# Kernel tuning notes

Measured on AMD Instinct MI355X. Metric: run time of the kernel, lower is better.

## Reference

```python
import jax, jax.numpy as jnp
import numpy as np

L, N, E, H = 1024, 8, 1024, 16
D = E // H

def setup_inputs() -> dict:
    key = jax.random.key(0)
    k1, k2, k3 = jax.random.split(key, 3)
    x = jax.random.normal(k1, (L, N, E), dtype=jnp.float32)
    # xavier-uniform-like scale for in_proj_weight (3E x E)
    bound = float(np.sqrt(6.0 / (3 * E + E)))
    in_proj_weight = jax.random.uniform(k2, (3 * E, E), dtype=jnp.float32, minval=-bound, maxval=bound)
    in_proj_bias = jnp.zeros((3 * E,), dtype=jnp.float32)
    wb = float(np.sqrt(1.0 / E))
    out_w = jax.random.uniform(k3, (E, E), dtype=jnp.float32, minval=-wb, maxval=wb)
    out_b = jnp.zeros((E,), dtype=jnp.float32)
    return {"x": x, "in_proj_weight": in_proj_weight, "in_proj_bias": in_proj_bias,
            "out_w": out_w, "out_b": out_b}

def reference(x, in_proj_weight, in_proj_bias, out_w, out_b):
    # self-attention: query == key == value == x, stacked input projection
    stack = x @ in_proj_weight.T + in_proj_bias          # L x N x 3E
    q, k, v = jnp.split(stack, 3, axis=-1)               # each L x N x E
    q = q.reshape(L, N, H, D)
    k = k.reshape(L, N, H, D)
    v = v.reshape(L, N, H, D)
    logit = jnp.einsum('lnhd,snhd->lnhs', q, k) / jnp.sqrt(jnp.float32(D))
    weight = jax.nn.softmax(logit, axis=-1)              # L x N x H x S
    context = jnp.einsum('lnhs,snhd->lnhd', weight, v)   # L x N x H x D
    context = context.reshape(L, N, E) @ out_w.T + out_b # L x N x E
    attn = jnp.transpose(weight.mean(axis=-2), (1, 0, 2))  # N x L x S
    return context, attn
```

## Files before the change

### kernel.cpp

```cpp
#include <hip/hip_runtime.h>
#include <stdint.h>

#define LL 1024
#define NB 8
#define EE 1024
#define HH 16
#define DD 64
#define MM (LL*NB)
#define K3 (3*EE)

typedef __attribute__((ext_vector_type(8))) short bf16x8;
typedef __attribute__((ext_vector_type(4))) float f32x4;
typedef __attribute__((ext_vector_type(4))) unsigned short u16x4;
typedef __attribute__((ext_vector_type(8))) unsigned short u16x8;

__device__ __forceinline__ unsigned short f2bf(float f) {
  uint32_t u = __builtin_bit_cast(uint32_t, f);
  u += 0x7fffu + ((u >> 16) & 1u);
  return (unsigned short)(u >> 16);
}
__device__ __forceinline__ uint32_t cvtpk(float lo, float hi) {
  uint32_t d;
  asm volatile("v_cvt_pk_bf16_f32 %0, %1, %2" : "=v"(d) : "v"(lo), "v"(hi));
  return d;
}
__device__ __forceinline__ f32x4 mfma16(bf16x8 a, bf16x8 b, f32x4 c) {
  return __builtin_amdgcn_mfma_f32_16x16x32_bf16(a, b, c, 0, 0, 0);
}
__device__ __forceinline__ void gload16(const unsigned short* src, unsigned short* dst) {
  __builtin_amdgcn_global_load_lds(
      (const __attribute__((address_space(1))) uint32_t*)src,
      (__attribute__((address_space(3))) uint32_t*)dst, 16, 0, 0);
}

__global__ void cvt3_kernel(const float* __restrict__ a, const float* __restrict__ b,
                            const float* __restrict__ c,
                            unsigned short* __restrict__ da, unsigned short* __restrict__ db,
                            unsigned short* __restrict__ dc) {
  const int NA = (MM * EE) / 4, NBq = (K3 * EE) / 4, NC = (EE * EE) / 4;
  const int total = NA + NBq + NC;
  for (int i = blockIdx.x * blockDim.x + threadIdx.x; i < total; i += gridDim.x * blockDim.x) {
    const float* s; unsigned short* d; int j;
    if (i < NA)            { s = a; d = da; j = i; }
    else if (i < NA + NBq) { s = b; d = db; j = i - NA; }
    else                   { s = c; d = dc; j = i - NA - NBq; }
    f32x4 v = ((const f32x4*)s)[j];
    u16x4 o;
    o[0] = f2bf(v[0]); o[1] = f2bf(v[1]); o[2] = f2bf(v[2]); o[3] = f2bf(v[3]);
    ((u16x4*)d)[j] = o;
  }
}

template<int MODE>
__global__ __launch_bounds__(256) void gemm_bt(
    const unsigned short* __restrict__ A, const unsigned short* __restrict__ B,
    const float* __restrict__ bias, float* __restrict__ Cf,
    unsigned short* __restrict__ qo, unsigned short* __restrict__ kto,
    unsigned short* __restrict__ vo)
{
  constexpr int NNc = (MODE == 1) ? 3072 : 1024;
  constexpr int BPX = NNc / 1024;
  constexpr int KD  = 1024;

  __shared__ __align__(16) unsigned short smem[16384];

  const int bid = blockIdx.x;
  const int xcd = bid & 7;
  const int t = bid >> 3;
  const int brow = t / BPX;
  const int bcol = xcd * BPX + t % BPX;

  const int tid = threadIdx.x;
  const int w = tid >> 6, lane = tid & 63;
  const int wr = w >> 1, wc = w & 1;
  const int lrow = lane & 15, g = lane >> 4;

  f32x4 acc[4][4];
#pragma unroll
  for (int i = 0; i < 4; ++i)
#pragma unroll
    for (int j = 0; j < 4; ++j) acc[i][j] = (f32x4){0.f, 0.f, 0.f, 0.f};

  const int r_in = lane >> 2;
  const int u = lane & 3;

  auto stage = [&](int kt) {
    unsigned short* a_lds = smem + ((kt & 1) ? 8192 : 0);
    unsigned short* b_lds = a_lds + 4096;
    const size_t kcol = (size_t)kt * 32 + u * 8;
    gload16(A + (size_t)(brow * 128 + 16 * w + r_in) * KD + kcol,       &a_lds[(16 * w) * 32]);
    gload16(A + (size_t)(brow * 128 + 16 * (w + 4) + r_in) * KD + kcol, &a_lds[(16 * (w + 4)) * 32]);
    gload16(B + (size_t)(bcol * 128 + 16 * w + r_in) * KD + kcol,       &b_lds[(16 * w) * 32]);
    gload16(B + (size_t)(bcol * 128 + 16 * (w + 4) + r_in) * KD + kcol, &b_lds[(16 * (w + 4)) * 32]);
  };

  const int KT = KD >> 5;
  stage(0);
  for (int kt = 0; kt < KT; ++kt) {
    __syncthreads();
    if (kt + 1 < KT) stage(kt + 1);
    const unsigned short* a_lds = smem + ((kt & 1) ? 8192 : 0);
    const unsigned short* b_lds = a_lds + 4096;
    bf16x8 af[4], bfr[4];
#pragma unroll
    for (int mt = 0; mt < 4; ++mt)
      af[mt] = *(const bf16x8*)&a_lds[(wr * 64 + mt * 16 + lrow) * 32 + g * 8];
#pragma unroll
    for (int nt = 0; nt < 4; ++nt)
      bfr[nt] = *(const bf16x8*)&b_lds[(wc * 64 + nt * 16 + lrow) * 32 + g * 8];
#pragma unroll
    for (int mt = 0; mt < 4; ++mt)
#pragma unroll
      for (int nt = 0; nt < 4; ++nt)
        acc[mt][nt] = mfma16(af[mt], bfr[nt], acc[mt][nt]);
  }

  if (MODE == 0) {
#pragma unroll
    for (int nt = 0; nt < 4; ++nt) {
      const int c = bcol * 128 + wc * 64 + nt * 16 + lrow;
      const float bv = bias[c];
#pragma unroll
      for (int mt = 0; mt < 4; ++mt) {
        const int m0 = brow * 128 + wr * 64 + mt * 16 + g * 4;
#pragma unroll
        for (int j = 0; j < 4; ++j)
          Cf[(size_t)(m0 + j) * NNc + c] = acc[mt][nt][j] + bv;
      }
    }
  } else {
    __syncthreads();
    const float qs = (bcol < 8) ? 0.125f : 1.0f;
#pragma unroll
    for (int nt = 0; nt < 4; ++nt) {
      const int c = bcol * 128 + wc * 64 + nt * 16 + lrow;
      const float bv = bias[c];
      const int lc = wc * 64 + nt * 16 + lrow;
#pragma unroll
      for (int mt = 0; mt < 4; ++mt) {
        const int lr0 = wr * 64 + mt * 16 + g * 4;
#pragma unroll
        for (int j = 0; j < 4; ++j)
          smem[(lr0 + j) * 128 + lc] = f2bf((acc[mt][nt][j] + bv) * qs);
      }
    }
    __syncthreads();
#pragma unroll
    for (int i = 0; i < 8; ++i) {
      const int unit = i * 256 + tid;
      const int r = unit >> 4, cu = unit & 15;
      const u16x8 val = *(const u16x8*)&smem[r * 128 + cu * 8];
      const int m = brow * 128 + r;
      const int c = bcol * 128 + cu * 8;
      const int region = c >> 10, cl = c & 1023;
      if (region == 0)      *(u16x8*)&qo[(size_t)m * EE + cl] = val;
      else if (region == 2) *(u16x8*)&vo[(size_t)m * EE + cl] = val;
      else *(u16x8*)&kto[((size_t)((m & 7) * HH + (cl >> 6)) * LL + (m >> 3)) * DD + (cl & 63)] = val;
    }
  }
}

__global__ void transpose_v(const unsigned short* __restrict__ v, unsigned short* __restrict__ vt) {
  __shared__ __align__(16) unsigned short tile[64][68];
  const int b = blockIdx.x;
  const int lchunk = b & 15, h = (b >> 4) & 15, n = b >> 8;
  const int t = threadIdx.x;
  const int c4 = (t & 15) * 4, r = t >> 4;
#pragma unroll
  for (int p = 0; p < 4; ++p) {
    const int l = lchunk * 64 + p * 16 + r;
    u16x4 x = *(const u16x4*)&v[(size_t)(l * NB + n) * EE + h * DD + c4];
    *(u16x4*)&tile[p * 16 + r][c4] = x;
  }
  __syncthreads();
#pragma unroll
  for (int p = 0; p < 4; ++p) {
    const int d = p * 16 + r;
    u16x4 o;
#pragma unroll
    for (int i = 0; i < 4; ++i) o[i] = tile[c4 + i][d];
    *(u16x4*)&vt[((size_t)(n * HH + h) * DD + d) * LL + lchunk * 64 + c4] = o;
  }
}

__global__ __launch_bounds__(256) void attn_flash(
    const unsigned short* __restrict__ q,
    const unsigned short* __restrict__ kt,
    const unsigned short* __restrict__ vt,
    unsigned short* __restrict__ ctxo,
    float* __restrict__ rinvb)
{
  __shared__ __align__(16) unsigned short kc[2][64][64];
  __shared__ __align__(16) unsigned short pl[4][4][16][72];

  const int bid = blockIdx.x;
  const int n = bid & 7;
  const int rest = bid >> 3;
  const int h = rest >> 2;
  const int lt = (rest & 3) << 8;
  const int tid = threadIdx.x;
  const int wv = tid >> 6, lane = tid & 63;
  const int ll = lane & 15, g = lane >> 4;
  const int a3 = ll & 7;

  bf16x8 qf0[4], qf1[4];
#pragma unroll
  for (int T = 0; T < 4; ++T) {
    const int lr = lt + T * 64 + wv * 16 + ll;
    const unsigned short* qp = q + ((size_t)lr * NB + n) * EE + h * DD + g * 8;
    qf0[T] = *(const bf16x8*)qp;
    qf1[T] = *(const bf16x8*)(qp + 32);
  }

  const unsigned short* kslab = kt + (size_t)(n * HH + h) * LL * DD;
  const unsigned short* vbase = vt + (size_t)(n * HH + h) * DD * LL;

  const int r8 = lane >> 3;
  const int c16 = (lane & 7) ^ r8;
  const int kof0 = ll * 128 + ((g ^ a3) << 4);
  const int kof1 = ll * 128 + (((4 + g) ^ a3) << 4);

  auto stageK = [&](int buf, int ch) {
    unsigned short* kd = &kc[buf][wv * 16][0];
    const unsigned short* src = kslab + (size_t)(ch * 64 + wv * 16) * DD;
    gload16(src + (size_t)r8 * DD + c16 * 8,       kd);
    gload16(src + (size_t)(8 + r8) * DD + c16 * 8, kd + 8 * 64);
  };

  f32x4 ctx[4][4];
  f32x4 sum[4];
#pragma unroll
  for (int T = 0; T < 4; ++T) {
    sum[T] = (f32x4){0.f, 0.f, 0.f, 0.f};
#pragma unroll
    for (int dt = 0; dt < 4; ++dt) ctx[T][dt] = (f32x4){0.f, 0.f, 0.f, 0.f};
  }

  char* plb = (char*)&pl[wv][0][0][0];

  stageK(0, 0);
  for (int ch = 0; ch < 16; ++ch) {
    __syncthreads();
    const int buf = ch & 1;
    const char* kb = (const char*)&kc[buf][0][0];

    bf16x8 vf0[4], vf1[4];
#pragma unroll
    for (int dt = 0; dt < 4; ++dt) {
      const unsigned short* vp = vbase + (size_t)(dt * 16 + ll) * LL + ch * 64 + g * 8;
      vf0[dt] = *(const bf16x8*)vp;
      vf1[dt] = *(const bf16x8*)(vp + 32);
    }
    if (ch < 15) stageK(buf ^ 1, ch + 1);

#pragma unroll
    for (int t = 0; t < 4; ++t) {
      const bf16x8 kf0 = *(const bf16x8*)(kb + t * 2048 + kof0);
      const bf16x8 kf1 = *(const bf16x8*)(kb + t * 2048 + kof1);
#pragma unroll
      for (int T = 0; T < 4; ++T) {
        f32x4 sc = (f32x4){0.f, 0.f, 0.f, 0.f};
        sc = mfma16(kf0, qf0[T], sc);
        sc = mfma16(kf1, qf1[T], sc);
        f32x4 p;
#pragma unroll
        for (int j = 0; j < 4; ++j) p[j] = __expf(sc[j]);
        sum[T] += p;
        uint2 wT; wT.x = cvtpk(p[0], p[1]); wT.y = cvtpk(p[2], p[3]);
        *(uint2*)(plb + T * 2304 + ll * 144 + (t * 16 + g * 4) * 2) = wT;
      }
    }
#pragma unroll
    for (int T = 0; T < 4; ++T) {
      const bf16x8 pf0 = *(const bf16x8*)(plb + T * 2304 + ll * 144 + g * 16);
      const bf16x8 pf1 = *(const bf16x8*)(plb + T * 2304 + ll * 144 + 64 + g * 16);
#pragma unroll
      for (int dt = 0; dt < 4; ++dt) {
        ctx[T][dt] = mfma16(vf0[dt], pf0, ctx[T][dt]);
        ctx[T][dt] = mfma16(vf1[dt], pf1, ctx[T][dt]);
      }
    }
  }

#pragma unroll
  for (int T = 0; T < 4; ++T) {
    float s1 = sum[T][0] + sum[T][1] + sum[T][2] + sum[T][3];
    s1 += __shfl_xor(s1, 16); s1 += __shfl_xor(s1, 32);
    const float rinv = 1.0f / s1;
    if (lane < 16) rinvb[(size_t)(n * HH + h) * LL + lt + T * 64 + wv * 16 + lane] = rinv;
    const int lr = lt + T * 64 + wv * 16 + ll;
    unsigned short* cp = ctxo + ((size_t)lr * NB + n) * EE + h * DD;
#pragma unroll
    for (int dt = 0; dt < 4; ++dt) {
      uint2 o;
      o.x = cvtpk(ctx[T][dt][0] * rinv, ctx[T][dt][1] * rinv);
      o.y = cvtpk(ctx[T][dt][2] * rinv, ctx[T][dt][3] * rinv);
      *(uint2*)(cp + dt * 16 + g * 4) = o;
    }
  }
}

__global__ __launch_bounds__(256) void attn_mean(
    const unsigned short* __restrict__ q,
    const unsigned short* __restrict__ kt,
    const float* __restrict__ rinvb,
    float* __restrict__ attn_out)
{
  __shared__ __align__(16) unsigned short kc[2][128][64];

  const int bid = blockIdx.x;
  const int n = bid & 7;
  const int r = bid >> 3;
  const int sh = r & 7;
  const int lt = (r >> 3) << 6;
  const int tid = threadIdx.x;
  const int wv = tid >> 6, lane = tid & 63;
  const int ll = lane & 15, g = lane >> 4;
  const int a3 = ll & 7;
  const int sb = sh << 7;
  const int lrow = lt + wv * 16 + ll;

  const int r8 = lane >> 3;
  const int c16 = (lane & 7) ^ r8;
  const int kof0 = ll * 128 + ((g ^ a3) << 4);
  const int kof1 = ll * 128 + (((4 + g) ^ a3) << 4);

  const unsigned short* kwin = kt + (size_t)n * HH * LL * DD + (size_t)sb * DD;

  auto stage = [&](int buf, int h) {
    unsigned short* kd = &kc[buf][wv * 32][0];
    const unsigned short* src = kwin + (size_t)h * LL * DD + (size_t)(wv * 32) * DD;
#pragma unroll
    for (int i = 0; i < 4; ++i)
      gload16(src + (size_t)(i * 8 + r8) * DD + c16 * 8, kd + i * 8 * 64);
  };

  float rv[16];
#pragma unroll
  for (int h = 0; h < HH; ++h) rv[h] = rinvb[(size_t)(n * HH + h) * LL + lrow];

  const unsigned short* qb2 = q + ((size_t)lrow * NB + n) * EE + g * 8;

  f32x4 acc[8];
#pragma unroll
  for (int i = 0; i < 8; ++i) acc[i] = (f32x4){0.f, 0.f, 0.f, 0.f};

  stage(0, 0);
  for (int h = 0; h < HH; ++h) {
    __syncthreads();
    const char* kb = (const char*)&kc[h & 1][0][0];
    const unsigned short* qp = qb2 + h * DD;
    const bf16x8 qf0 = *(const bf16x8*)qp;
    const bf16x8 qf1 = *(const bf16x8*)(qp + 32);
    if (h + 1 < HH) stage((h + 1) & 1, h + 1);
    const float rvh = rv[h];
#pragma unroll
    for (int t = 0; t < 8; ++t) {
      bf16x8 kf0 = *(const bf16x8*)(kb + t * 2048 + kof0);
      bf16x8 kf1 = *(const bf16x8*)(kb + t * 2048 + kof1);
      f32x4 sc = (f32x4){0.f, 0.f, 0.f, 0.f};
      sc = mfma16(kf0, qf0, sc);
      sc = mfma16(kf1, qf1, sc);
#pragma unroll
      for (int j = 0; j < 4; ++j) acc[t][j] += __expf(sc[j]) * rvh;
    }
  }

  float* ap = attn_out + ((size_t)n * LL + lrow) * LL + sb + g * 4;
#pragma unroll
  for (int t = 0; t < 8; ++t) *(f32x4*)(ap + t * 16) = acc[t] * 0.0625f;
}

extern "C" void kernel_launch(void* const* d_in, const int* in_sizes, int n_in,
                              void* d_out, int out_size, void* d_ws, size_t ws_size,
                              hipStream_t stream) {
  const float* x   = (const float*)d_in[0];
  const float* win = (const float*)d_in[1];
  const float* bin = (const float*)d_in[2];
  const float* ow  = (const float*)d_in[3];
  const float* ob  = (const float*)d_in[4];
  float* out = (float*)d_out;

  const size_t need = ((size_t)MM * EE * 5 + (size_t)K3 * EE + (size_t)EE * EE) * 2
                    + (size_t)NB * HH * LL * 4;
  if (ws_size < need) return;

  unsigned short* ws  = (unsigned short*)d_ws;
  unsigned short* xb  = ws;
  unsigned short* wb  = xb + (size_t)MM * EE;
  unsigned short* owb = wb + (size_t)K3 * EE;
  unsigned short* qb  = owb + (size_t)EE * EE;
  unsigned short* ktb = qb + (size_t)MM * EE;
  unsigned short* vb  = ktb + (size_t)MM * EE;
  unsigned short* vtb = vb + (size_t)MM * EE;
  float* rinvb = (float*)(vtb + (size_t)MM * EE);
  unsigned short* ctx = xb;

  cvt3_kernel<<<2048, 256, 0, stream>>>(x, win, ow, xb, wb, owb);
  gemm_bt<1><<<64 * (K3 / 128), 256, 0, stream>>>(xb, wb, bin, nullptr, qb, ktb, vb);
  transpose_v<<<2048, 256, 0, stream>>>(vb, vtb);
  attn_flash<<<512, 256, 0, stream>>>(qb, ktb, vtb, ctx, rinvb);
  attn_mean<<<1024, 256, 0, stream>>>(qb, ktb, rinvb, out + (size_t)MM * EE);
  gemm_bt<0><<<64 * (EE / 128), 256, 0, stream>>>(ctx, owb, ob, out, nullptr, nullptr, nullptr);
}
```

Before: 207.6 us.

## Widen GEMM tile to 128x256 and remap workgroups across XCDs

Doubles the N dimension of each GEMM block tile so each wave computes 64x128 outputs with 32 accumulators, raising A-operand reuse per LDS load. Workgroup IDs are remapped so consecutive tiles land on the same XCD, and the launch bounds now request two blocks per CU. The trade-off is higher register and LDS use and half as many blocks, which may leave CUs underfilled for the output projection.

```diff
diff --git a/kernel.cpp b/kernel.cpp
--- a/kernel.cpp
+++ b/kernel.cpp
@@ -52,46 +52,49 @@
 }
 
 template<int MODE>
-__global__ __launch_bounds__(256) void gemm_bt(
+__global__ __launch_bounds__(256, 2) void gemm_bt(
     const unsigned short* __restrict__ A, const unsigned short* __restrict__ B,
     const float* __restrict__ bias, float* __restrict__ Cf,
     unsigned short* __restrict__ qo, unsigned short* __restrict__ kto,
     unsigned short* __restrict__ vo)
 {
   constexpr int NNc = (MODE == 1) ? 3072 : 1024;
-  constexpr int BPX = NNc / 1024;
+  constexpr int BPC = NNc / 256;
   constexpr int KD  = 1024;
-
-  __shared__ __align__(16) unsigned short smem[16384];
+  constexpr int SMEM = (MODE == 1) ? 33280 : 24576;
+  __shared__ __align__(16) unsigned short smem[SMEM];
 
   const int bid = blockIdx.x;
-  const int xcd = bid & 7;
-  const int t = bid >> 3;
-  const int brow = t / BPX;
-  const int bcol = xcd * BPX + t % BPX;
+  const int q8 = gridDim.x >> 3;
+  const int wgid = (bid & 7) * q8 + (bid >> 3);
+  const int brow = wgid / BPC;
+  const int bcol = wgid % BPC;
 
   const int tid = threadIdx.x;
   const int w = tid >> 6, lane = tid & 63;
   const int wr = w >> 1, wc = w & 1;
   const int lrow = lane & 15, g = lane >> 4;
 
-  f32x4 acc[4][4];
+  f32x4 acc[4][8];
 #pragma unroll
   for (int i = 0; i < 4; ++i)
 #pragma unroll
-    for (int j = 0; j < 4; ++j) acc[i][j] = (f32x4){0.f, 0.f, 0.f, 0.f};
+    for (int j = 0; j < 8; ++j) acc[i][j] = (f32x4){0.f, 0.f, 0.f, 0.f};
 
   const int r_in = lane >> 2;
   const int u = lane & 3;
 
   auto stage = [&](int kt) {
-    unsigned short* a_lds = smem + ((kt & 1) ? 8192 : 0);
-    unsigned short* b_lds = a_lds + 4096;
+    unsigned short* base = smem + ((kt & 1) ? 12288 : 0);
+    unsigned short* a_lds = base;
+    unsigned short* b_lds = base + 4096;
     const size_t kcol = (size_t)kt * 32 + u * 8;
     gload16(A + (size_t)(brow * 128 + 16 * w + r_in) * KD + kcol,       &a_lds[(16 * w) * 32]);
     gload16(A + (size_t)(brow * 128 + 16 * (w + 4) + r_in) * KD + kcol, &a_lds[(16 * (w + 4)) * 32]);
-    gload16(B + (size_t)(bcol * 128 + 16 * w + r_in) * KD + kcol,       &b_lds[(16 * w) * 32]);
-    gload16(B + (size_t)(bcol * 128 + 16 * (w + 4) + r_in) * KD + kcol, &b_lds[(16 * (w + 4)) * 32]);
+#pragma unroll
+    for (int i = 0; i < 4; ++i)
+      gload16(B + (size_t)(bcol * 256 + 16 * (w + 4 * i) + r_in) * KD + kcol,
+              &b_lds[(16 * (w + 4 * i)) * 32]);
   };
 
   const int KT = KD >> 5;
@@ -99,26 +102,27 @@
   for (int kt = 0; kt < KT; ++kt) {
     __syncthreads();
     if (kt + 1 < KT) stage(kt + 1);
-    const unsigned short* a_lds = smem + ((kt & 1) ? 8192 : 0);
-    const unsigned short* b_lds = a_lds + 4096;
-    bf16x8 af[4], bfr[4];
+    const unsigned short* base = smem + ((kt & 1) ? 12288 : 0);
+    const unsigned short* a_lds = base;
+    const unsigned short* b_lds = base + 4096;
+    bf16x8 af[4], bfr[8];
 #pragma unroll
     for (int mt = 0; mt < 4; ++mt)
       af[mt] = *(const bf16x8*)&a_lds[(wr * 64 + mt * 16 + lrow) * 32 + g * 8];
 #pragma unroll
-    for (int nt = 0; nt < 4; ++nt)
-      bfr[nt] = *(const bf16x8*)&b_lds[(wc * 64 + nt * 16 + lrow) * 32 + g * 8];
+    for (int nt = 0; nt < 8; ++nt)
+      bfr[nt] = *(const bf16x8*)&b_lds[(wc * 128 + nt * 16 + lrow) * 32 + g * 8];
 #pragma unroll
     for (int mt = 0; mt < 4; ++mt)
 #pragma unroll
-      for (int nt = 0; nt < 4; ++nt)
+      for (int nt = 0; nt < 8; ++nt)
         acc[mt][nt] = mfma16(af[mt], bfr[nt], acc[mt][nt]);
   }
 
   if (MODE == 0) {
 #pragma unroll
-    for (int nt = 0; nt < 4; ++nt) {
-      const int c = bcol * 128 + wc * 64 + nt * 16 + lrow;
+    for (int nt = 0; nt < 8; ++nt) {
+      const int c = bcol * 256 + wc * 128 + nt * 16 + lrow;
       const float bv = bias[c];
 #pragma unroll
       for (int mt = 0; mt < 4; ++mt) {
@@ -130,28 +134,28 @@
     }
   } else {
     __syncthreads();
-    const float qs = (bcol < 8) ? 0.125f : 1.0f;
-#pragma unroll
-    for (int nt = 0; nt < 4; ++nt) {
-      const int c = bcol * 128 + wc * 64 + nt * 16 + lrow;
+    const float qs = (bcol < 4) ? 0.125f : 1.0f;
+#pragma unroll
+    for (int nt = 0; nt < 8; ++nt) {
+      const int c = bcol * 256 + wc * 128 + nt * 16 + lrow;
       const float bv = bias[c];
-      const int lc = wc * 64 + nt * 16 + lrow;
+      const int lc = wc * 128 + nt * 16 + lrow;
 #pragma unroll
       for (int mt = 0; mt < 4; ++mt) {
         const int lr0 = wr * 64 + mt * 16 + g * 4;
 #pragma unroll
         for (int j = 0; j < 4; ++j)
-          smem[(lr0 + j) * 128 + lc] = f2bf((acc[mt][nt][j] + bv) * qs);
+          smem[(lr0 + j) * 260 + lc] = f2bf((acc[mt][nt][j] + bv) * qs);
       }
     }
     __syncthreads();
 #pragma unroll
-    for (int i = 0; i < 8; ++i) {
+    for (int i = 0; i < 16; ++i) {
       const int unit = i * 256 + tid;
-      const int r = unit >> 4, cu = unit & 15;
-      const u16x8 val = *(const u16x8*)&smem[r * 128 + cu * 8];
+      const int r = unit >> 5, cu = unit & 31;
+      const u16x8 val = *(const u16x8*)&smem[r * 260 + cu * 8];
       const int m = brow * 128 + r;
-      const int c = bcol * 128 + cu * 8;
+      const int c = bcol * 256 + cu * 8;
       const int region = c >> 10, cl = c & 1023;
       if (region == 0)      *(u16x8*)&qo[(size_t)m * EE + cl] = val;
       else if (region == 2) *(u16x8*)&vo[(size_t)m * EE + cl] = val;
@@ -397,9 +401,9 @@
   unsigned short* ctx = xb;
 
   cvt3_kernel<<<2048, 256, 0, stream>>>(x, win, ow, xb, wb, owb);
-  gemm_bt<1><<<64 * (K3 / 128), 256, 0, stream>>>(xb, wb, bin, nullptr, qb, ktb, vb);
+  gemm_bt<1><<<64 * (K3 / 256), 256, 0, stream>>>(xb, wb, bin, nullptr, qb, ktb, vb);
   transpose_v<<<2048, 256, 0, stream>>>(vb, vtb);
   attn_flash<<<512, 256, 0, stream>>>(qb, ktb, vtb, ctx, rinvb);
   attn_mean<<<1024, 256, 0, stream>>>(qb, ktb, rinvb, out + (size_t)MM * EE);
-  gemm_bt<0><<<64 * (EE / 128), 256, 0, stream>>>(ctx, owb, ob, out, nullptr, nullptr, nullptr);
-}
+  gemm_bt<0><<<64 * (EE / 256), 256, 0, stream>>>(ctx, owb, ob, out, nullptr, nullptr, nullptr);
+}
```

Result: no change. 203.6 us (-2.0%).

## Merge attention-mean and output-projection GEMM into one launch

Applied to the files above, without the earlier changes.

Combines the attn_mean kernel and the output projection GEMM into a single launch of 1536 blocks. The first 1024 blocks compute the head-averaged attention weights and the remaining 512 compute ctx @ out_w^T + bias, each with its own staging. This removes one kernel launch and its tail, and lets the two independent workloads share the GPU at once. The cost is a branchy kernel whose register and LDS budget is set by the larger path. The gemm template is also specialised into a dedicated input-projection kernel.

```diff
diff --git a/kernel.cpp b/kernel.cpp
--- a/kernel.cpp
+++ b/kernel.cpp
@@ -51,15 +51,13 @@
   }
 }
 
-template<int MODE>
-__global__ __launch_bounds__(256) void gemm_bt(
+__global__ __launch_bounds__(256) void gemm_in(
     const unsigned short* __restrict__ A, const unsigned short* __restrict__ B,
-    const float* __restrict__ bias, float* __restrict__ Cf,
+    const float* __restrict__ bias,
     unsigned short* __restrict__ qo, unsigned short* __restrict__ kto,
     unsigned short* __restrict__ vo)
 {
-  constexpr int NNc = (MODE == 1) ? 3072 : 1024;
-  constexpr int BPX = NNc / 1024;
+  constexpr int BPX = 3;
   constexpr int KD  = 1024;
 
   __shared__ __align__(16) unsigned short smem[16384];
@@ -115,48 +113,33 @@
         acc[mt][nt] = mfma16(af[mt], bfr[nt], acc[mt][nt]);
   }
 
-  if (MODE == 0) {
-#pragma unroll
-    for (int nt = 0; nt < 4; ++nt) {
-      const int c = bcol * 128 + wc * 64 + nt * 16 + lrow;
-      const float bv = bias[c];
-#pragma unroll
-      for (int mt = 0; mt < 4; ++mt) {
-        const int m0 = brow * 128 + wr * 64 + mt * 16 + g * 4;
-#pragma unroll
-        for (int j = 0; j < 4; ++j)
-          Cf[(size_t)(m0 + j) * NNc + c] = acc[mt][nt][j] + bv;
-      }
-    }
-  } else {
-    __syncthreads();
-    const float qs = (bcol < 8) ? 0.125f : 1.0f;
-#pragma unroll
-    for (int nt = 0; nt < 4; ++nt) {
-      const int c = bcol * 128 + wc * 64 + nt * 16 + lrow;
-      const float bv = bias[c];
-      const int lc = wc * 64 + nt * 16 + lrow;
-#pragma unroll
-      for (int mt = 0; mt < 4; ++mt) {
-        const int lr0 = wr * 64 + mt * 16 + g * 4;
-#pragma unroll
-        for (int j = 0; j < 4; ++j)
-          smem[(lr0 + j) * 128 + lc] = f2bf((acc[mt][nt][j] + bv) * qs);
-      }
-    }
-    __syncthreads();
-#pragma unroll
-    for (int i = 0; i < 8; ++i) {
-      const int unit = i * 256 + tid;
-      const int r = unit >> 4, cu = unit & 15;
-      const u16x8 val = *(const u16x8*)&smem[r * 128 + cu * 8];
-      const int m = brow * 128 + r;
-      const int c = bcol * 128 + cu * 8;
-      const int region = c >> 10, cl = c & 1023;
-      if (region == 0)      *(u16x8*)&qo[(size_t)m * EE + cl] = val;
-      else if (region == 2) *(u16x8*)&vo[(size_t)m * EE + cl] = val;
-      else *(u16x8*)&kto[((size_t)((m & 7) * HH + (cl >> 6)) * LL + (m >> 3)) * DD + (cl & 63)] = val;
-    }
+  __syncthreads();
+  const float qs = (bcol < 8) ? 0.125f : 1.0f;
+#pragma unroll
+  for (int nt = 0; nt < 4; ++nt) {
+    const int c = bcol * 128 + wc * 64 + nt * 16 + lrow;
+    const float bv = bias[c];
+    const int lc = wc * 64 + nt * 16 + lrow;
+#pragma unroll
+    for (int mt = 0; mt < 4; ++mt) {
+      const int lr0 = wr * 64 + mt * 16 + g * 4;
+#pragma unroll
+      for (int j = 0; j < 4; ++j)
+        smem[(lr0 + j) * 128 + lc] = f2bf((acc[mt][nt][j] + bv) * qs);
+    }
+  }
+  __syncthreads();
+#pragma unroll
+  for (int i = 0; i < 8; ++i) {
+    const int unit = i * 256 + tid;
+    const int r = unit >> 4, cu = unit & 15;
+    const u16x8 val = *(const u16x8*)&smem[r * 128 + cu * 8];
+    const int m = brow * 128 + r;
+    const int c = bcol * 128 + cu * 8;
+    const int region = c >> 10, cl = c & 1023;
+    if (region == 0)      *(u16x8*)&qo[(size_t)m * EE + cl] = val;
+    else if (region == 2) *(u16x8*)&vo[(size_t)m * EE + cl] = val;
+    else *(u16x8*)&kto[((size_t)((m & 7) * HH + (cl >> 6)) * LL + (m >> 3)) * DD + (cl & 63)] = val;
   }
 }
 
@@ -300,75 +283,145 @@
   }
 }
 
-__global__ __launch_bounds__(256) void attn_mean(
+__global__ __launch_bounds__(256) void mean_out(
     const unsigned short* __restrict__ q,
     const unsigned short* __restrict__ kt,
     const float* __restrict__ rinvb,
-    float* __restrict__ attn_out)
+    float* __restrict__ attn_out,
+    const unsigned short* __restrict__ ctx,
+    const unsigned short* __restrict__ ow,
+    const float* __restrict__ ob,
+    float* __restrict__ out)
 {
-  __shared__ __align__(16) unsigned short kc[2][128][64];
+  __shared__ __align__(16) unsigned short smem[16384];
 
   const int bid = blockIdx.x;
-  const int n = bid & 7;
-  const int r = bid >> 3;
-  const int sh = r & 7;
-  const int lt = (r >> 3) << 6;
   const int tid = threadIdx.x;
   const int wv = tid >> 6, lane = tid & 63;
   const int ll = lane & 15, g = lane >> 4;
-  const int a3 = ll & 7;
-  const int sb = sh << 7;
-  const int lrow = lt + wv * 16 + ll;
-
-  const int r8 = lane >> 3;
-  const int c16 = (lane & 7) ^ r8;
-  const int kof0 = ll * 128 + ((g ^ a3) << 4);
-  const int kof1 = ll * 128 + (((4 + g) ^ a3) << 4);
-
-  const unsigned short* kwin = kt + (size_t)n * HH * LL * DD + (size_t)sb * DD;
-
-  auto stage = [&](int buf, int h) {
-    unsigned short* kd = &kc[buf][wv * 32][0];
-    const unsigned short* src = kwin + (size_t)h * LL * DD + (size_t)(wv * 32) * DD;
+
+  if (bid < 1024) {
+    unsigned short (*kc)[128][64] = (unsigned short (*)[128][64])smem;
+    const int n = bid & 7;
+    const int r = bid >> 3;
+    const int sh = r & 7;
+    const int lt = (r >> 3) << 6;
+    const int a3 = ll & 7;
+    const int sb = sh << 7;
+    const int lrow = lt + wv * 16 + ll;
+
+    const int r8 = lane >> 3;
+    const int c16 = (lane & 7) ^ r8;
+    const int kof0 = ll * 128 + ((g ^ a3) << 4);
+    const int kof1 = ll * 128 + (((4 + g) ^ a3) << 4);
+
+    const unsigned short* kwin = kt + (size_t)n * HH * LL * DD + (size_t)sb * DD;
+
+    auto stage = [&](int buf, int h) {
+      unsigned short* kd = &kc[buf][wv * 32][0];
+      const unsigned short* src = kwin + (size_t)h * LL * DD + (size_t)(wv * 32) * DD;
+#pragma unroll
+      for (int i = 0; i < 4; ++i)
+        gload16(src + (size_t)(i * 8 + r8) * DD + c16 * 8, kd + i * 8 * 64);
+    };
+
+    float rv[16];
+#pragma unroll
+    for (int h = 0; h < HH; ++h) rv[h] = rinvb[(size_t)(n * HH + h) * LL + lrow];
+
+    const unsigned short* qb2 = q + ((size_t)lrow * NB + n) * EE + g * 8;
+
+    f32x4 acc[8];
+#pragma unroll
+    for (int i = 0; i < 8; ++i) acc[i] = (f32x4){0.f, 0.f, 0.f, 0.f};
+
+    stage(0, 0);
+    for (int h = 0; h < HH; ++h) {
+      __syncthreads();
+      const char* kb = (const char*)&kc[h & 1][0][0];
+      const unsigned short* qp = qb2 + h * DD;
+      const bf16x8 qf0 = *(const bf16x8*)qp;
+      const bf16x8 qf1 = *(const bf16x8*)(qp + 32);
+      if (h + 1 < HH) stage((h + 1) & 1, h + 1);
+      const float rvh = rv[h];
+#pragma unroll
+      for (int t = 0; t < 8; ++t) {
+        bf16x8 kf0 = *(const bf16x8*)(kb + t * 2048 + kof0);
+        bf16x8 kf1 = *(const bf16x8*)(kb + t * 2048 + kof1);
+        f32x4 sc = (f32x4){0.f, 0.f, 0.f, 0.f};
+        sc = mfma16(kf0, qf0, sc);
+        sc = mfma16(kf1, qf1, sc);
+#pragma unroll
+        for (int j = 0; j < 4; ++j) acc[t][j] += __expf(sc[j]) * rvh;
+      }
+    }
+
+    float* ap = attn_out + ((size_t)n * LL + lrow) * LL + sb + g * 4;
+#pragma unroll
+    for (int t = 0; t < 8; ++t) *(f32x4*)(ap + t * 16) = acc[t] * 0.0625f;
+
+  } else {
+    const int b2 = bid - 1024;
+    const int wgid = (b2 & 7) * 64 + (b2 >> 3);
+    const int brow = wgid & 63;
+    const int bcol = wgid >> 6;
+
+    const int w = wv;
+    const int wr = w >> 1, wc = w & 1;
+    const int lrow = ll;
+
+    f32x4 acc[4][4];
 #pragma unroll
     for (int i = 0; i < 4; ++i)
-      gload16(src + (size_t)(i * 8 + r8) * DD + c16 * 8, kd + i * 8 * 64);
-  };
-
-  float rv[16];
-#pragma unroll
-  for (int h = 0; h < HH; ++h) rv[h] = rinvb[(size_t)(n * HH + h) * LL + lrow];
-
-  const unsigned short* qb2 = q + ((size_t)lrow * NB + n) * EE + g * 8;
-
-  f32x4 acc[8];
-#pragma unroll
-  for (int i = 0; i < 8; ++i) acc[i] = (f32x4){0.f, 0.f, 0.f, 0.f};
-
-  stage(0, 0);
-  for (int h = 0; h < HH; ++h) {
-    __syncthreads();
-    const char* kb = (const char*)&kc[h & 1][0][0];
-    const unsigned short* qp = qb2 + h * DD;
-    const bf16x8 qf0 = *(const bf16x8*)qp;
-    const bf16x8 qf1 = *(const bf16x8*)(qp + 32);
-    if (h + 1 < HH) stage((h + 1) & 1, h + 1);
-    const float rvh = rv[h];
-#pragma unroll
-    for (int t = 0; t < 8; ++t) {
-      bf16x8 kf0 = *(const bf16x8*)(kb + t * 2048 + kof0);
-      bf16x8 kf1 = *(const bf16x8*)(kb + t * 2048 + kof1);
-      f32x4 sc = (f32x4){0.f, 0.f, 0.f, 0.f};
-      sc = mfma16(kf0, qf0, sc);
-      sc = mfma16(kf1, qf1, sc);
-#pragma unroll
-      for (int j = 0; j < 4; ++j) acc[t][j] += __expf(sc[j]) * rvh;
-    }
-  }
-
-  float* ap = attn_out + ((size_t)n * LL + lrow) * LL + sb + g * 4;
-#pragma unroll
-  for (int t = 0; t < 8; ++t) *(f32x4*)(ap + t * 16) = acc[t] * 0.0625f;
+#pragma unroll
+      for (int j = 0; j < 4; ++j) acc[i][j] = (f32x4){0.f, 0.f, 0.f, 0.f};
+
+    const int r_in = lane >> 2;
+    const int u = lane & 3;
+
+    auto stage = [&](int kt2) {
+      unsigned short* a_lds = smem + ((kt2 & 1) ? 8192 : 0);
+      unsigned short* b_lds = a_lds + 4096;
+      const size_t kcol = (size_t)kt2 * 32 + u * 8;
+      gload16(ctx + (size_t)(brow * 128 + 16 * w + r_in) * 1024 + kcol,       &a_lds[(16 * w) * 32]);
+      gload16(ctx + (size_t)(brow * 128 + 16 * (w + 4) + r_in) * 1024 + kcol, &a_lds[(16 * (w + 4)) * 32]);
+      gload16(ow + (size_t)(bcol * 128 + 16 * w + r_in) * 1024 + kcol,        &b_lds[(16 * w) * 32]);
+      gload16(ow + (size_t)(bcol * 128 + 16 * (w + 4) + r_in) * 1024 + kcol,  &b_lds[(16 * (w + 4)) * 32]);
+    };
+
+    stage(0);
+    for (int kt2 = 0; kt2 < 32; ++kt2) {
+      __syncthreads();
+      if (kt2 + 1 < 32) stage(kt2 + 1);
+      const unsigned short* a_lds = smem + ((kt2 & 1) ? 8192 : 0);
+      const unsigned short* b_lds = a_lds + 4096;
+      bf16x8 af[4], bfr[4];
+#pragma unroll
+      for (int mt = 0; mt < 4; ++mt)
+        af[mt] = *(const bf16x8*)&a_lds[(wr * 64 + mt * 16 + lrow) * 32 + g * 8];
+#pragma unroll
+      for (int nt = 0; nt < 4; ++nt)
+        bfr[nt] = *(const bf16x8*)&b_lds[(wc * 64 + nt * 16 + lrow) * 32 + g * 8];
+#pragma unroll
+      for (int mt = 0; mt < 4; ++mt)
+#pragma unroll
+        for (int nt = 0; nt < 4; ++nt)
+          acc[mt][nt] = mfma16(af[mt], bfr[nt], acc[mt][nt]);
+    }
+
+#pragma unroll
+    for (int nt = 0; nt < 4; ++nt) {
+      const int c = bcol * 128 + wc * 64 + nt * 16 + lrow;
+      const float bv = ob[c];
+#pragma unroll
+      for (int mt = 0; mt < 4; ++mt) {
+        const int m0 = brow * 128 + wr * 64 + mt * 16 + g * 4;
+#pragma unroll
+        for (int j = 0; j < 4; ++j)
+          out[(size_t)(m0 + j) * 1024 + c] = acc[mt][nt][j] + bv;
+      }
+    }
+  }
 }
 
 extern "C" void kernel_launch(void* const* d_in, const int* in_sizes, int n_in,
@@ -397,9 +450,9 @@
   unsigned short* ctx = xb;
 
   cvt3_kernel<<<2048, 256, 0, stream>>>(x, win, ow, xb, wb, owb);
-  gemm_bt<1><<<64 * (K3 / 128), 256, 0, stream>>>(xb, wb, bin, nullptr, qb, ktb, vb);
+  gemm_in<<<1536, 256, 0, stream>>>(xb, wb, bin, qb, ktb, vb);
   transpose_v<<<2048, 256, 0, stream>>>(vb, vtb);
   attn_flash<<<512, 256, 0, stream>>>(qb, ktb, vtb, ctx, rinvb);
-  attn_mean<<<1024, 256, 0, stream>>>(qb, ktb, rinvb, out + (size_t)MM * EE);
-  gemm_bt<0><<<64 * (EE / 128), 256, 0, stream>>>(ctx, owb, ob, out, nullptr, nullptr, nullptr);
-}
+  mean_out<<<1536, 256, 0, stream>>>(qb, ktb, rinvb, out + (size_t)MM * EE,
+                                     ctx, owb, ob, out);
+}
```

Result: faster. 203.1 us, median of 2 (-2.2%).
